# Kernel optimization log

Measured on AMD Instinct MI355X. Metric: run time of the kernel, lower is better.

## Reference

```python
import jax, jax.numpy as jnp
import numpy as np

B, C, E = 2, 128, 60000

def conv1(x, W, b):
    # pointwise conv1d: x [B,Cin,E], W [Cout,Cin], b [Cout] -> [B,Cout,E]
    return jnp.einsum('oc,bce->boe', W, x) + b[None, :, None]

def mesh_conv(x, gi, W, b):
    # MeshCNN GeMM conv: x [B,C,E], gi [B,E,4] neighbor edge ids, W [Cout,Cin,5], b [Cout]
    f = jax.vmap(lambda xb, ib: xb[:, ib])(x, gi)  # [B,C,E,4] neighbor gather
    f1, f2, f3, f4 = f[..., 0], f[..., 1], f[..., 2], f[..., 3]
    # symmetric features: [e, a+c, b+d, |a-c|, |b-d|]
    G = jnp.stack([x, f1 + f3, f2 + f4, jnp.abs(f1 - f3), jnp.abs(f2 - f4)], axis=-1)  # [B,C,E,5]
    return jnp.einsum('bces,ocs->boe', G, W) + b[None, :, None]


def setup_inputs() -> dict:
    key = jax.random.key(0)
    ks = jax.random.split(key, 16)
    s = 0.05
    return {
        'x_0': jax.random.normal(ks[0], (B, C, E), jnp.float32),
        'x_1': jax.random.normal(ks[1], (B, C, E), jnp.float32),
        'gemm': jax.random.randint(ks[2], (B, E, 4), 0, E, jnp.int32),
        'Wa_local': jax.random.normal(ks[3], (C, C), jnp.float32) * s,
        'ba_local': jax.random.normal(ks[4], (C,), jnp.float32) * s,
        'Wb_local': jax.random.normal(ks[5], (C, C), jnp.float32) * s,
        'bb_local': jax.random.normal(ks[6], (C,), jnp.float32) * s,
        'Wa_tri': jax.random.normal(ks[7], (C, C, 5), jnp.float32) * s,
        'ba_tri': jax.random.normal(ks[8], (C,), jnp.float32) * s,
        'Wb_tri': jax.random.normal(ks[9], (C, C, 5), jnp.float32) * s,
        'bb_tri': jax.random.normal(ks[10], (C,), jnp.float32) * s,
        'Wa_fuse': jax.random.normal(ks[11], (3, 2 * C), jnp.float32) * s,
        'ba_fuse': jax.random.normal(ks[12], (3,), jnp.float32) * s,
        'Wb_fuse': jax.random.normal(ks[13], (3, 2 * C), jnp.float32) * s,
        'bb_fuse': jax.random.normal(ks[14], (3,), jnp.float32) * s,
    }


def reference(x_0, x_1, gemm, Wa_local, ba_local, Wb_local, bb_local,
              Wa_tri, ba_tri, Wb_tri, bb_tri,
              Wa_fuse, ba_fuse, Wb_fuse, bb_fuse):
    a_local = conv1(x_0, Wa_local, ba_local)              # [B,C,E]
    a_tri = mesh_conv(x_0, gemm, Wa_tri, ba_tri)          # [B,C,E]
    x_a_two = jnp.concatenate([a_local, a_tri], axis=1)   # [B,2C,E]
    b_local = conv1(x_1, Wb_local, bb_local)
    b_tri = mesh_conv(x_1, gemm, Wb_tri, bb_tri)
    x_b_two = jnp.concatenate([b_local, b_tri], axis=1)
    x_a_w = conv1(x_a_two, Wa_fuse, ba_fuse)[:, None]     # [B,1,3,E]
    x_b_w = conv1(x_b_two, Wb_fuse, bb_fuse)[:, None]     # [B,1,3,E]
    return x_a_w + x_b_w
```

## Files before the change

### kernel.cpp

```cpp
#include <hip/hip_runtime.h>
#include <hip/hip_bf16.h>
#include <cstdint>

#define B_ 2
#define C_ 128
#define E_ 60000

typedef unsigned int uint32_;
typedef unsigned short ushort_;
typedef float v2f __attribute__((ext_vector_type(2)));

__device__ __forceinline__ v2f bp2(uint32_ v) {
    v2f r;
    r.x = __uint_as_float(v << 16);
    r.y = __uint_as_float(v & 0xffff0000u);
    return r;
}

__device__ __forceinline__ v2f vabs2(v2f a) {
    v2f r; r.x = fabsf(a.x); r.y = fabsf(a.y); return r;
}

__device__ __forceinline__ ushort_ f2b(float f) {
    union { float f; uint32_ u; } x; x.f = f;
    uint32_ u = x.u + 0x7fffu + ((x.u >> 16) & 1u);
    return (ushort_)(u >> 16);
}

__device__ __forceinline__ float swz_add(float v, const int pat) {
    switch (pat) {
    case 1:  return v + __int_as_float(__builtin_amdgcn_ds_swizzle(__float_as_int(v), 0x041F));
    case 2:  return v + __int_as_float(__builtin_amdgcn_ds_swizzle(__float_as_int(v), 0x081F));
    case 4:  return v + __int_as_float(__builtin_amdgcn_ds_swizzle(__float_as_int(v), 0x101F));
    case 8:  return v + __int_as_float(__builtin_amdgcn_ds_swizzle(__float_as_int(v), 0x201F));
    default: return v + __int_as_float(__builtin_amdgcn_ds_swizzle(__float_as_int(v), 0x401F));
    }
}

__global__ __launch_bounds__(256) void prep_kernel(
    const float* __restrict__ x0, const float* __restrict__ x1,
    const float* __restrict__ Wa_local, const float* __restrict__ ba_local,
    const float* __restrict__ Wb_local, const float* __restrict__ bb_local,
    const float* __restrict__ Wa_tri,  const float* __restrict__ ba_tri,
    const float* __restrict__ Wb_tri,  const float* __restrict__ bb_tri,
    const float* __restrict__ Wa_fuse, const float* __restrict__ ba_fuse,
    const float* __restrict__ Wb_fuse, const float* __restrict__ bb_fuse,
    ushort_* __restrict__ xt, float* __restrict__ Vw, float* __restrict__ cst)
{
    __shared__ float smem[32 * 65];
    const int lane = threadIdx.x & 63;
    const int wv   = threadIdx.x >> 6;

    if (blockIdx.x < 60) {
        const int pj    = blockIdx.x / 10;
        const int chunk = blockIdx.x % 10;
        const int p = pj / 3, j = pj % 3;
        const int f = chunk * 64 + lane;
        const float* Wf = p ? Wb_fuse : Wa_fuse;
        const float* Wt = p ? Wb_tri  : Wa_tri;
        const float* Wl = p ? Wb_local : Wa_local;
        const int o0 = wv * 32;
        float a0 = 0.f, a1 = 0.f, a2 = 0.f, a3 = 0.f;
        for (int o = o0; o < o0 + 32; o += 4) {
            a0 += Wf[j * 256 + 128 + o]     * Wt[(o)     * 640 + f];
            a1 += Wf[j * 256 + 129 + o]     * Wt[(o + 1) * 640 + f];
            a2 += Wf[j * 256 + 130 + o]     * Wt[(o + 2) * 640 + f];
            a3 += Wf[j * 256 + 131 + o]     * Wt[(o + 3) * 640 + f];
        }
        float acc = (a0 + a1) + (a2 + a3);
        const int s = f % 5, c = f / 5;
        if (s == 0) {
            float b0 = 0.f, b1 = 0.f, b2 = 0.f, b3 = 0.f;
            for (int o = o0; o < o0 + 32; o += 4) {
                b0 += Wf[j * 256 + o]     * Wl[(o)     * C_ + c];
                b1 += Wf[j * 256 + o + 1] * Wl[(o + 1) * C_ + c];
                b2 += Wf[j * 256 + o + 2] * Wl[(o + 2) * C_ + c];
                b3 += Wf[j * 256 + o + 3] * Wl[(o + 3) * C_ + c];
            }
            acc += (b0 + b1) + (b2 + b3);
        }
        smem[wv * 64 + lane] = acc;
        __syncthreads();
        if (wv == 0) {
            float tot = smem[lane] + smem[64 + lane] + smem[128 + lane] + smem[192 + lane];
            Vw[(pj * 5 + s) * C_ + c] = tot;
        }
    } else if (blockIdx.x == 60) {
        const int j = wv;
        if (j < 3) {
            float acc;
            {
                const int l = lane;
                acc = Wa_fuse[j * 256 + l]       * ba_local[l]
                    + Wa_fuse[j * 256 + 128 + l] * ba_tri[l]
                    + Wb_fuse[j * 256 + l]       * bb_local[l]
                    + Wb_fuse[j * 256 + 128 + l] * bb_tri[l];
            }
            {
                const int l = lane + 64;
                acc += Wa_fuse[j * 256 + l]       * ba_local[l]
                     + Wa_fuse[j * 256 + 128 + l] * ba_tri[l]
                     + Wb_fuse[j * 256 + l]       * bb_local[l]
                     + Wb_fuse[j * 256 + 128 + l] * bb_tri[l];
            }
            acc = swz_add(acc, 1); acc = swz_add(acc, 2); acc = swz_add(acc, 4);
            acc = swz_add(acc, 8); acc = swz_add(acc, 16);
            acc += __shfl_xor(acc, 32, 64);
            if (lane == 0) cst[j] = acc + ba_fuse[j] + bb_fuse[j];
        }
    } else {
        const int tb = blockIdx.x - 61;
        const int bx = tb % 1875;
        const int rz = tb / 1875;
        const int by = rz & 1;
        const int bz = rz >> 1;
        const int which = bz >> 1;
        const int b     = bz & 1;
        const float* src = (which ? x1 : x0) + (size_t)b * C_ * E_;
        const int e0 = bx * 32;
        const int c0 = by * 64;
        const int t  = threadIdx.x;
        float (*tile)[65] = (float(*)[65])smem;
        {
            const int c  = t >> 2;
            const int e8 = (t & 3) * 8;
            const float* pp = src + (size_t)(c0 + c) * E_ + e0 + e8;
            float4 v0 = *(const float4*)pp;
            float4 v1 = *(const float4*)(pp + 4);
            tile[e8 + 0][c] = v0.x; tile[e8 + 1][c] = v0.y;
            tile[e8 + 2][c] = v0.z; tile[e8 + 3][c] = v0.w;
            tile[e8 + 4][c] = v1.x; tile[e8 + 5][c] = v1.y;
            tile[e8 + 6][c] = v1.z; tile[e8 + 7][c] = v1.w;
        }
        __syncthreads();
        {
            const int e  = t >> 3;
            const int c8 = (t & 7) * 8;
            const float* r = &tile[e][c8];
            uint32_ w0 = (uint32_)f2b(r[0]) | ((uint32_)f2b(r[1]) << 16);
            uint32_ w1 = (uint32_)f2b(r[2]) | ((uint32_)f2b(r[3]) << 16);
            uint32_ w2 = (uint32_)f2b(r[4]) | ((uint32_)f2b(r[5]) << 16);
            uint32_ w3 = (uint32_)f2b(r[6]) | ((uint32_)f2b(r[7]) << 16);
            uint4 w; w.x = w0; w.y = w1; w.z = w2; w.w = w3;
            const size_t rec = (size_t)((b * E_ + e0 + e) * 2 + which);
            *(uint4*)(xt + (rec << 7) + c0 + c8) = w;
        }
    }
}

struct GD {
    uint32_ A0, A1, A2, A3, A4;
    uint32_ Cc0, Cc1, Cc2, Cc3, Cc4;
    uint32_ D0, D1, D2, D3, D4;
    uint32_ F0, F1, F2, F3, F4;
};

__device__ __forceinline__ GD issue_loads(const uint32_* __restrict__ xt,
                                          int pair, int4 gA, int4 gB, int lane)
{
    const int e0 = 2 * pair;
    const uint32_ badd = (e0 >= E_) ? (uint32_)E_ : 0u;
    const uint32_ sA = ((uint32_)e0 << 7) + lane;
    const uint32_ sB = sA + 128;
    const uint32_ n1 = ((badd + (uint32_)gA.x) << 7) + lane;
    const uint32_ n2 = ((badd + (uint32_)gA.y) << 7) + lane;
    const uint32_ n3 = ((badd + (uint32_)gA.z) << 7) + lane;
    const uint32_ n4 = ((badd + (uint32_)gA.w) << 7) + lane;
    const uint32_ m1 = ((badd + (uint32_)gB.x) << 7) + lane;
    const uint32_ m2 = ((badd + (uint32_)gB.y) << 7) + lane;
    const uint32_ m3 = ((badd + (uint32_)gB.z) << 7) + lane;
    const uint32_ m4 = ((badd + (uint32_)gB.w) << 7) + lane;
    GD g;
    g.A0 = xt[sA]; g.Cc0 = xt[sA + 64];
    g.A1 = xt[n1]; g.Cc1 = xt[n1 + 64];
    g.A2 = xt[n2]; g.Cc2 = xt[n2 + 64];
    g.A3 = xt[n3]; g.Cc3 = xt[n3 + 64];
    g.A4 = xt[n4]; g.Cc4 = xt[n4 + 64];
    g.D0 = xt[sB]; g.F0 = xt[sB + 64];
    g.D1 = xt[m1]; g.F1 = xt[m1 + 64];
    g.D2 = xt[m2]; g.F2 = xt[m2 + 64];
    g.D3 = xt[m3]; g.F3 = xt[m3 + 64];
    g.D4 = xt[m4]; g.F4 = xt[m4 + 64];
    return g;
}

__device__ __forceinline__ void edge3(uint32_ X0, uint32_ X1, uint32_ X2, uint32_ X3, uint32_ X4,
                                      uint32_ Y0, uint32_ Y1, uint32_ Y2, uint32_ Y3, uint32_ Y4,
                                      const v2f (*w)[3][5],
                                      float& r0, float& r1, float& r2)
{
    v2f a0 = bp2(X0), a1 = bp2(X1), a2 = bp2(X2), a3 = bp2(X3), a4 = bp2(X4);
    v2f b0 = bp2(Y0), b1 = bp2(Y1), b2 = bp2(Y2), b3 = bp2(Y3), b4 = bp2(Y4);
    v2f sa1 = a1 + a3, sa2 = a2 + a4;
    v2f da1 = vabs2(a1 - a3), da2 = vabs2(a2 - a4);
    v2f sb1 = b1 + b3, sb2 = b2 + b4;
    v2f db1 = vabs2(b1 - b3), db2 = vabs2(b2 - b4);
    v2f t0 = w[0][0][0] * a0, t1 = w[0][1][0] * a0, t2 = w[0][2][0] * a0;
    t0 += w[0][0][1] * sa1; t1 += w[0][1][1] * sa1; t2 += w[0][2][1] * sa1;
    t0 += w[0][0][2] * sa2; t1 += w[0][1][2] * sa2; t2 += w[0][2][2] * sa2;
    t0 += w[0][0][3] * da1; t1 += w[0][1][3] * da1; t2 += w[0][2][3] * da1;
    t0 += w[0][0][4] * da2; t1 += w[0][1][4] * da2; t2 += w[0][2][4] * da2;
    t0 += w[1][0][0] * b0;  t1 += w[1][1][0] * b0;  t2 += w[1][2][0] * b0;
    t0 += w[1][0][1] * sb1; t1 += w[1][1][1] * sb1; t2 += w[1][2][1] * sb1;
    t0 += w[1][0][2] * sb2; t1 += w[1][1][2] * sb2; t2 += w[1][2][2] * sb2;
    t0 += w[1][0][3] * db1; t1 += w[1][1][3] * db1; t2 += w[1][2][3] * db1;
    t0 += w[1][0][4] * db2; t1 += w[1][1][4] * db2; t2 += w[1][2][4] * db2;
    r0 = t0.x + t0.y; r1 = t1.x + t1.y; r2 = t2.x + t2.y;
}

__global__ __launch_bounds__(256, 3) void mesh_fused_kernel(
    const uint32_* __restrict__ xt, const int* __restrict__ gemm,
    const float* __restrict__ Vw, const float* __restrict__ cst,
    float* __restrict__ out)
{
    const int lane = threadIdx.x & 63;
    const int wv   = threadIdx.x >> 6;
    const int gw   = blockIdx.x * 4 + wv;
    const int nw   = gridDim.x * 4;

    v2f w[2][3][5];
#pragma unroll
    for (int p = 0; p < 2; ++p)
#pragma unroll
        for (int j = 0; j < 3; ++j)
#pragma unroll
            for (int s = 0; s < 5; ++s)
                w[p][j][s] = *(const v2f*)(Vw + (((p * 3 + j) * 5 + s) << 7) + lane * 2);

    const int  jj     = lane >> 4;
    const bool is0    = (jj == 0), is1 = (jj == 1);
    const bool writer = ((lane & 15) == 0) && (jj < 3);
    const float cj    = is0 ? cst[0] : (is1 ? cst[1] : cst[2]);
    float* obase      = out + (size_t)(jj < 3 ? jj : 2) * E_;

    const int4* g4 = (const int4*)gemm;
    const int npair = (B_ * E_) / 2;

    int pnext = (gw + nw < npair) ? gw + nw : gw;
    int4 giA = g4[2 * gw], giB = g4[2 * gw + 1];
    GD cur = issue_loads(xt, gw, giA, giB, lane);
    int4 niA = g4[2 * pnext], niB = g4[2 * pnext + 1];

#pragma unroll 2
    for (int pair = gw; pair < npair; pair += nw) {
        GD nb = issue_loads(xt, pnext, niA, niB, lane);
        const int p2 = (pnext + nw < npair) ? pnext + nw : pnext;
        niA = g4[2 * p2]; niB = g4[2 * p2 + 1];

        float rA0, rA1, rA2, rB0, rB1, rB2;
        edge3(cur.A0, cur.A1, cur.A2, cur.A3, cur.A4,
              cur.Cc0, cur.Cc1, cur.Cc2, cur.Cc3, cur.Cc4, w, rA0, rA1, rA2);
        edge3(cur.D0, cur.D1, cur.D2, cur.D3, cur.D4,
              cur.F0, cur.F1, cur.F2, cur.F3, cur.F4, w, rB0, rB1, rB2);

        rA0 = swz_add(rA0, 16); rB0 = swz_add(rB0, 16);
        rA1 = swz_add(rA1, 16); rB1 = swz_add(rB1, 16);
        rA2 = swz_add(rA2, 16); rB2 = swz_add(rB2, 16);
        rA0 += __shfl_xor(rA0, 32, 64); rB0 += __shfl_xor(rB0, 32, 64);
        rA1 += __shfl_xor(rA1, 32, 64); rB1 += __shfl_xor(rB1, 32, 64);
        rA2 += __shfl_xor(rA2, 32, 64); rB2 += __shfl_xor(rB2, 32, 64);

        float vA = is0 ? rA0 : (is1 ? rA1 : rA2);
        float vB = is0 ? rB0 : (is1 ? rB1 : rB2);
        vA = swz_add(vA, 1); vB = swz_add(vB, 1);
        vA = swz_add(vA, 2); vB = swz_add(vB, 2);
        vA = swz_add(vA, 4); vB = swz_add(vB, 4);
        vA = swz_add(vA, 8); vB = swz_add(vB, 8);

        if (writer) {
            const int e0p = 2 * pair;
            const int bb  = (e0p >= E_) ? 1 : 0;
            const int ee  = e0p - (bb ? E_ : 0);
            float2 st; st.x = vA + cj; st.y = vB + cj;
            *(float2*)(obase + (bb ? 3 * E_ : 0) + ee) = st;
        }

        cur = nb;
        pnext = p2;
    }
}

extern "C" void kernel_launch(void* const* d_in, const int* in_sizes, int n_in,
                              void* d_out, int out_size, void* d_ws, size_t ws_size,
                              hipStream_t stream) {
    const float* x0       = (const float*)d_in[0];
    const float* x1       = (const float*)d_in[1];
    const int*   gemm     = (const int*)d_in[2];
    const float* Wa_local = (const float*)d_in[3];
    const float* ba_local = (const float*)d_in[4];
    const float* Wb_local = (const float*)d_in[5];
    const float* bb_local = (const float*)d_in[6];
    const float* Wa_tri   = (const float*)d_in[7];
    const float* ba_tri   = (const float*)d_in[8];
    const float* Wb_tri   = (const float*)d_in[9];
    const float* bb_tri   = (const float*)d_in[10];
    const float* Wa_fuse  = (const float*)d_in[11];
    const float* ba_fuse  = (const float*)d_in[12];
    const float* Wb_fuse  = (const float*)d_in[13];
    const float* bb_fuse  = (const float*)d_in[14];
    float* out = (float*)d_out;

    ushort_* xt  = (ushort_*)d_ws;
    float*   Vw  = (float*)(xt + (size_t)B_ * E_ * 2 * C_);
    float*   cst = Vw + 2 * 3 * 5 * C_;

    hipLaunchKernelGGL(prep_kernel, dim3(61 + 15000), dim3(256), 0, stream,
                       x0, x1,
                       Wa_local, ba_local, Wb_local, bb_local,
                       Wa_tri, ba_tri, Wb_tri, bb_tri,
                       Wa_fuse, ba_fuse, Wb_fuse, bb_fuse, xt, Vw, cst);

    hipLaunchKernelGGL(mesh_fused_kernel, dim3(2048), dim3(256), 0, stream,
                       (const uint32_*)xt, gemm, Vw, cst, out);
}
```

Before: 214.8 us.

## Restructure transpose blocks to cover both inputs and all channels per tile

The prep transpose now has each block handle 32 edges across all 128 channels of both x0 and x1, converting to bf16 before staging in shared memory with a padded row stride. Each block then writes whole 512-byte records with four 16-byte stores. This cuts the block count from 15000 to 3750 and halves shared-memory traffic, at the cost of strided 128-byte global reads per thread. A sched_barrier is also added in the main loop to keep prefetch loads from being interleaved with compute.

```diff
diff --git a/kernel.cpp b/kernel.cpp
--- a/kernel.cpp
+++ b/kernel.cpp
@@ -36,6 +36,8 @@
     default: return v + __int_as_float(__builtin_amdgcn_ds_swizzle(__float_as_int(v), 0x401F));
     }
 }
+
+#define RS_ 264
 
 __global__ __launch_bounds__(256) void prep_kernel(
     const float* __restrict__ x0, const float* __restrict__ x1,
@@ -47,11 +49,12 @@
     const float* __restrict__ Wb_fuse, const float* __restrict__ bb_fuse,
     ushort_* __restrict__ xt, float* __restrict__ Vw, float* __restrict__ cst)
 {
-    __shared__ float smem[32 * 65];
+    __shared__ __align__(16) ushort_ smem_us[32 * RS_];
     const int lane = threadIdx.x & 63;
     const int wv   = threadIdx.x >> 6;
 
     if (blockIdx.x < 60) {
+        float* smemf = (float*)smem_us;
         const int pj    = blockIdx.x / 10;
         const int chunk = blockIdx.x % 10;
         const int p = pj / 3, j = pj % 3;
@@ -79,10 +82,10 @@
             }
             acc += (b0 + b1) + (b2 + b3);
         }
-        smem[wv * 64 + lane] = acc;
+        smemf[wv * 64 + lane] = acc;
         __syncthreads();
         if (wv == 0) {
-            float tot = smem[lane] + smem[64 + lane] + smem[128 + lane] + smem[192 + lane];
+            float tot = smemf[lane] + smemf[64 + lane] + smemf[128 + lane] + smemf[192 + lane];
             Vw[(pj * 5 + s) * C_ + c] = tot;
         }
     } else if (blockIdx.x == 60) {
@@ -110,41 +113,36 @@
         }
     } else {
         const int tb = blockIdx.x - 61;
+        const int b  = tb / 1875;
         const int bx = tb % 1875;
-        const int rz = tb / 1875;
-        const int by = rz & 1;
-        const int bz = rz >> 1;
-        const int which = bz >> 1;
-        const int b     = bz & 1;
-        const float* src = (which ? x1 : x0) + (size_t)b * C_ * E_;
         const int e0 = bx * 32;
-        const int c0 = by * 64;
         const int t  = threadIdx.x;
-        float (*tile)[65] = (float(*)[65])smem;
-        {
-            const int c  = t >> 2;
-            const int e8 = (t & 3) * 8;
-            const float* pp = src + (size_t)(c0 + c) * E_ + e0 + e8;
-            float4 v0 = *(const float4*)pp;
-            float4 v1 = *(const float4*)(pp + 4);
-            tile[e8 + 0][c] = v0.x; tile[e8 + 1][c] = v0.y;
-            tile[e8 + 2][c] = v0.z; tile[e8 + 3][c] = v0.w;
-            tile[e8 + 4][c] = v1.x; tile[e8 + 5][c] = v1.y;
-            tile[e8 + 6][c] = v1.z; tile[e8 + 7][c] = v1.w;
+        const int which = t >> 7;
+        const int c     = t & 127;
+        const float* src = (which ? x1 : x0) + ((size_t)b * C_ + c) * E_ + e0;
+        float4 v[8];
+#pragma unroll
+        for (int k = 0; k < 8; ++k) v[k] = ((const float4*)src)[k];
+#pragma unroll
+        for (int k = 0; k < 8; ++k) {
+            smem_us[(4 * k + 0) * RS_ + t] = f2b(v[k].x);
+            smem_us[(4 * k + 1) * RS_ + t] = f2b(v[k].y);
+            smem_us[(4 * k + 2) * RS_ + t] = f2b(v[k].z);
+            smem_us[(4 * k + 3) * RS_ + t] = f2b(v[k].w);
         }
         __syncthreads();
-        {
-            const int e  = t >> 3;
-            const int c8 = (t & 7) * 8;
-            const float* r = &tile[e][c8];
-            uint32_ w0 = (uint32_)f2b(r[0]) | ((uint32_)f2b(r[1]) << 16);
-            uint32_ w1 = (uint32_)f2b(r[2]) | ((uint32_)f2b(r[3]) << 16);
-            uint32_ w2 = (uint32_)f2b(r[4]) | ((uint32_)f2b(r[5]) << 16);
-            uint32_ w3 = (uint32_)f2b(r[6]) | ((uint32_)f2b(r[7]) << 16);
-            uint4 w; w.x = w0; w.y = w1; w.z = w2; w.w = w3;
-            const size_t rec = (size_t)((b * E_ + e0 + e) * 2 + which);
-            *(uint4*)(xt + (rec << 7) + c0 + c8) = w;
-        }
+        const int e  = t >> 3;
+        const int u0 = (t & 7) * 32;
+        const ushort_* r = smem_us + e * RS_ + u0;
+        uint4 w0 = *(const uint4*)(r);
+        uint4 w1 = *(const uint4*)(r + 8);
+        uint4 w2 = *(const uint4*)(r + 16);
+        uint4 w3 = *(const uint4*)(r + 24);
+        ushort_* dst = xt + ((size_t)(b * E_ + e0 + e) << 8) + u0;
+        ((uint4*)dst)[0] = w0;
+        ((uint4*)dst)[1] = w1;
+        ((uint4*)dst)[2] = w2;
+        ((uint4*)dst)[3] = w3;
     }
 }
 
@@ -247,6 +245,8 @@
         const int p2 = (pnext + nw < npair) ? pnext + nw : pnext;
         niA = g4[2 * p2]; niB = g4[2 * p2 + 1];
 
+        __builtin_amdgcn_sched_barrier(0);
+
         float rA0, rA1, rA2, rB0, rB1, rB2;
         edge3(cur.A0, cur.A1, cur.A2, cur.A3, cur.A4,
               cur.Cc0, cur.Cc1, cur.Cc2, cur.Cc3, cur.Cc4, w, rA0, rA1, rA2);
@@ -304,7 +304,7 @@
     float*   Vw  = (float*)(xt + (size_t)B_ * E_ * 2 * C_);
     float*   cst = Vw + 2 * 3 * 5 * C_;
 
-    hipLaunchKernelGGL(prep_kernel, dim3(61 + 15000), dim3(256), 0, stream,
+    hipLaunchKernelGGL(prep_kernel, dim3(61 + 2 * (E_ / 32)), dim3(256), 0, stream,
                        x0, x1,
                        Wa_local, ba_local, Wb_local, bb_local,
                        Wa_tri, ba_tri, Wb_tri, bb_tri,
```

Result: slower. 225.0 us (+4.7%).

## Split bf16 transposed features into channel halves and gather in two passes

Applied to the files above, without the earlier changes.

The bf16 transposed feature buffer is split into two channel halves (lo/hi), each holding 64 channels for both inputs per edge. The fused gather kernel becomes a half kernel launched twice: the first pass writes partial outputs and the second adds its contribution plus the constant. Each pass has half the working set, so random neighbor gathers are more likely to hit in cache. Each wave now handles four edges per iteration without software prefetch. The cost is an extra launch, a read-modify-write of the output, and a second read of the gather indices.

```diff
diff --git a/kernel.cpp b/kernel.cpp
--- a/kernel.cpp
+++ b/kernel.cpp
@@ -45,7 +45,8 @@
     const float* __restrict__ Wb_tri,  const float* __restrict__ bb_tri,
     const float* __restrict__ Wa_fuse, const float* __restrict__ ba_fuse,
     const float* __restrict__ Wb_fuse, const float* __restrict__ bb_fuse,
-    ushort_* __restrict__ xt, float* __restrict__ Vw, float* __restrict__ cst)
+    ushort_* __restrict__ xt_lo, ushort_* __restrict__ xt_hi,
+    float* __restrict__ Vw, float* __restrict__ cst)
 {
     __shared__ float smem[32 * 65];
     const int lane = threadIdx.x & 63;
@@ -117,6 +118,7 @@
         const int which = bz >> 1;
         const int b     = bz & 1;
         const float* src = (which ? x1 : x0) + (size_t)b * C_ * E_;
+        ushort_* half_base = by ? xt_hi : xt_lo;
         const int e0 = bx * 32;
         const int c0 = by * 64;
         const int t  = threadIdx.x;
@@ -142,90 +144,29 @@
             uint32_ w2 = (uint32_)f2b(r[4]) | ((uint32_)f2b(r[5]) << 16);
             uint32_ w3 = (uint32_)f2b(r[6]) | ((uint32_)f2b(r[7]) << 16);
             uint4 w; w.x = w0; w.y = w1; w.z = w2; w.w = w3;
-            const size_t rec = (size_t)((b * E_ + e0 + e) * 2 + which);
-            *(uint4*)(xt + (rec << 7) + c0 + c8) = w;
+            const size_t rec = (size_t)(b * E_ + e0 + e) * 2 + which;
+            *(uint4*)(half_base + (rec << 6) + c8) = w;
         }
     }
 }
 
-struct GD {
-    uint32_ A0, A1, A2, A3, A4;
-    uint32_ Cc0, Cc1, Cc2, Cc3, Cc4;
-    uint32_ D0, D1, D2, D3, D4;
-    uint32_ F0, F1, F2, F3, F4;
-};
-
-__device__ __forceinline__ GD issue_loads(const uint32_* __restrict__ xt,
-                                          int pair, int4 gA, int4 gB, int lane)
-{
-    const int e0 = 2 * pair;
-    const uint32_ badd = (e0 >= E_) ? (uint32_)E_ : 0u;
-    const uint32_ sA = ((uint32_)e0 << 7) + lane;
-    const uint32_ sB = sA + 128;
-    const uint32_ n1 = ((badd + (uint32_)gA.x) << 7) + lane;
-    const uint32_ n2 = ((badd + (uint32_)gA.y) << 7) + lane;
-    const uint32_ n3 = ((badd + (uint32_)gA.z) << 7) + lane;
-    const uint32_ n4 = ((badd + (uint32_)gA.w) << 7) + lane;
-    const uint32_ m1 = ((badd + (uint32_)gB.x) << 7) + lane;
-    const uint32_ m2 = ((badd + (uint32_)gB.y) << 7) + lane;
-    const uint32_ m3 = ((badd + (uint32_)gB.z) << 7) + lane;
-    const uint32_ m4 = ((badd + (uint32_)gB.w) << 7) + lane;
-    GD g;
-    g.A0 = xt[sA]; g.Cc0 = xt[sA + 64];
-    g.A1 = xt[n1]; g.Cc1 = xt[n1 + 64];
-    g.A2 = xt[n2]; g.Cc2 = xt[n2 + 64];
-    g.A3 = xt[n3]; g.Cc3 = xt[n3 + 64];
-    g.A4 = xt[n4]; g.Cc4 = xt[n4 + 64];
-    g.D0 = xt[sB]; g.F0 = xt[sB + 64];
-    g.D1 = xt[m1]; g.F1 = xt[m1 + 64];
-    g.D2 = xt[m2]; g.F2 = xt[m2 + 64];
-    g.D3 = xt[m3]; g.F3 = xt[m3 + 64];
-    g.D4 = xt[m4]; g.F4 = xt[m4 + 64];
-    return g;
-}
-
-__device__ __forceinline__ void edge3(uint32_ X0, uint32_ X1, uint32_ X2, uint32_ X3, uint32_ X4,
-                                      uint32_ Y0, uint32_ Y1, uint32_ Y2, uint32_ Y3, uint32_ Y4,
-                                      const v2f (*w)[3][5],
-                                      float& r0, float& r1, float& r2)
-{
-    v2f a0 = bp2(X0), a1 = bp2(X1), a2 = bp2(X2), a3 = bp2(X3), a4 = bp2(X4);
-    v2f b0 = bp2(Y0), b1 = bp2(Y1), b2 = bp2(Y2), b3 = bp2(Y3), b4 = bp2(Y4);
-    v2f sa1 = a1 + a3, sa2 = a2 + a4;
-    v2f da1 = vabs2(a1 - a3), da2 = vabs2(a2 - a4);
-    v2f sb1 = b1 + b3, sb2 = b2 + b4;
-    v2f db1 = vabs2(b1 - b3), db2 = vabs2(b2 - b4);
-    v2f t0 = w[0][0][0] * a0, t1 = w[0][1][0] * a0, t2 = w[0][2][0] * a0;
-    t0 += w[0][0][1] * sa1; t1 += w[0][1][1] * sa1; t2 += w[0][2][1] * sa1;
-    t0 += w[0][0][2] * sa2; t1 += w[0][1][2] * sa2; t2 += w[0][2][2] * sa2;
-    t0 += w[0][0][3] * da1; t1 += w[0][1][3] * da1; t2 += w[0][2][3] * da1;
-    t0 += w[0][0][4] * da2; t1 += w[0][1][4] * da2; t2 += w[0][2][4] * da2;
-    t0 += w[1][0][0] * b0;  t1 += w[1][1][0] * b0;  t2 += w[1][2][0] * b0;
-    t0 += w[1][0][1] * sb1; t1 += w[1][1][1] * sb1; t2 += w[1][2][1] * sb1;
-    t0 += w[1][0][2] * sb2; t1 += w[1][1][2] * sb2; t2 += w[1][2][2] * sb2;
-    t0 += w[1][0][3] * db1; t1 += w[1][1][3] * db1; t2 += w[1][2][3] * db1;
-    t0 += w[1][0][4] * db2; t1 += w[1][1][4] * db2; t2 += w[1][2][4] * db2;
-    r0 = t0.x + t0.y; r1 = t1.x + t1.y; r2 = t2.x + t2.y;
-}
-
-__global__ __launch_bounds__(256, 3) void mesh_fused_kernel(
-    const uint32_* __restrict__ xt, const int* __restrict__ gemm,
+__global__ __launch_bounds__(256, 3) void mesh_half_kernel(
+    const uint32_* __restrict__ xh, const int* __restrict__ gemm,
     const float* __restrict__ Vw, const float* __restrict__ cst,
-    float* __restrict__ out)
+    float* __restrict__ out, const int coff, const int finalp)
 {
     const int lane = threadIdx.x & 63;
     const int wv   = threadIdx.x >> 6;
     const int gw   = blockIdx.x * 4 + wv;
     const int nw   = gridDim.x * 4;
 
-    v2f w[2][3][5];
-#pragma unroll
-    for (int p = 0; p < 2; ++p)
-#pragma unroll
-        for (int j = 0; j < 3; ++j)
-#pragma unroll
-            for (int s = 0; s < 5; ++s)
-                w[p][j][s] = *(const v2f*)(Vw + (((p * 3 + j) * 5 + s) << 7) + lane * 2);
+    const int p = lane >> 5;
+    v2f w[3][5];
+#pragma unroll
+    for (int j = 0; j < 3; ++j)
+#pragma unroll
+        for (int s = 0; s < 5; ++s)
+            w[j][s] = *(const v2f*)(Vw + ((p * 3 + j) * 5 + s) * C_ + coff + (lane & 31) * 2);
 
     const int  jj     = lane >> 4;
     const bool is0    = (jj == 0), is1 = (jj == 1);
@@ -234,49 +175,80 @@
     float* obase      = out + (size_t)(jj < 3 ? jj : 2) * E_;
 
     const int4* g4 = (const int4*)gemm;
-    const int npair = (B_ * E_) / 2;
-
-    int pnext = (gw + nw < npair) ? gw + nw : gw;
-    int4 giA = g4[2 * gw], giB = g4[2 * gw + 1];
-    GD cur = issue_loads(xt, gw, giA, giB, lane);
-    int4 niA = g4[2 * pnext], niB = g4[2 * pnext + 1];
-
-#pragma unroll 2
-    for (int pair = gw; pair < npair; pair += nw) {
-        GD nb = issue_loads(xt, pnext, niA, niB, lane);
-        const int p2 = (pnext + nw < npair) ? pnext + nw : pnext;
-        niA = g4[2 * p2]; niB = g4[2 * p2 + 1];
-
-        float rA0, rA1, rA2, rB0, rB1, rB2;
-        edge3(cur.A0, cur.A1, cur.A2, cur.A3, cur.A4,
-              cur.Cc0, cur.Cc1, cur.Cc2, cur.Cc3, cur.Cc4, w, rA0, rA1, rA2);
-        edge3(cur.D0, cur.D1, cur.D2, cur.D3, cur.D4,
-              cur.F0, cur.F1, cur.F2, cur.F3, cur.F4, w, rB0, rB1, rB2);
-
-        rA0 = swz_add(rA0, 16); rB0 = swz_add(rB0, 16);
-        rA1 = swz_add(rA1, 16); rB1 = swz_add(rB1, 16);
-        rA2 = swz_add(rA2, 16); rB2 = swz_add(rB2, 16);
-        rA0 += __shfl_xor(rA0, 32, 64); rB0 += __shfl_xor(rB0, 32, 64);
-        rA1 += __shfl_xor(rA1, 32, 64); rB1 += __shfl_xor(rB1, 32, 64);
-        rA2 += __shfl_xor(rA2, 32, 64); rB2 += __shfl_xor(rB2, 32, 64);
-
-        float vA = is0 ? rA0 : (is1 ? rA1 : rA2);
-        float vB = is0 ? rB0 : (is1 ? rB1 : rB2);
-        vA = swz_add(vA, 1); vB = swz_add(vB, 1);
-        vA = swz_add(vA, 2); vB = swz_add(vB, 2);
-        vA = swz_add(vA, 4); vB = swz_add(vB, 4);
-        vA = swz_add(vA, 8); vB = swz_add(vB, 8);
+    const int nquad = (B_ * E_) / 4;
+
+    for (int q = gw; q < nquad; q += nw) {
+        const int e0g = 4 * q;
+        const int b   = (e0g >= E_) ? 1 : 0;
+        const uint32_ badd = b ? (uint32_)E_ : 0u;
+
+        const int4 g0 = g4[e0g], g1 = g4[e0g + 1], g2 = g4[e0g + 2], g3 = g4[e0g + 3];
+
+        uint32_ S[4], N1[4], N2[4], N3[4], N4[4];
+#pragma unroll
+        for (int k = 0; k < 4; ++k)
+            S[k] = xh[(((uint32_)(e0g + k)) << 6) + lane];
+        N1[0] = xh[((badd + (uint32_)g0.x) << 6) + lane];
+        N2[0] = xh[((badd + (uint32_)g0.y) << 6) + lane];
+        N3[0] = xh[((badd + (uint32_)g0.z) << 6) + lane];
+        N4[0] = xh[((badd + (uint32_)g0.w) << 6) + lane];
+        N1[1] = xh[((badd + (uint32_)g1.x) << 6) + lane];
+        N2[1] = xh[((badd + (uint32_)g1.y) << 6) + lane];
+        N3[1] = xh[((badd + (uint32_)g1.z) << 6) + lane];
+        N4[1] = xh[((badd + (uint32_)g1.w) << 6) + lane];
+        N1[2] = xh[((badd + (uint32_)g2.x) << 6) + lane];
+        N2[2] = xh[((badd + (uint32_)g2.y) << 6) + lane];
+        N3[2] = xh[((badd + (uint32_)g2.z) << 6) + lane];
+        N4[2] = xh[((badd + (uint32_)g2.w) << 6) + lane];
+        N1[3] = xh[((badd + (uint32_)g3.x) << 6) + lane];
+        N2[3] = xh[((badd + (uint32_)g3.y) << 6) + lane];
+        N3[3] = xh[((badd + (uint32_)g3.z) << 6) + lane];
+        N4[3] = xh[((badd + (uint32_)g3.w) << 6) + lane];
+
+        float r0[4], r1[4], r2[4];
+#pragma unroll
+        for (int k = 0; k < 4; ++k) {
+            v2f a0 = bp2(S[k]);
+            v2f a1 = bp2(N1[k]), a2 = bp2(N2[k]), a3 = bp2(N3[k]), a4 = bp2(N4[k]);
+            v2f s1 = a1 + a3, s2 = a2 + a4;
+            v2f d1 = vabs2(a1 - a3), d2 = vabs2(a2 - a4);
+            v2f t0 = w[0][0] * a0, t1 = w[1][0] * a0, t2 = w[2][0] * a0;
+            t0 += w[0][1] * s1; t1 += w[1][1] * s1; t2 += w[2][1] * s1;
+            t0 += w[0][2] * s2; t1 += w[1][2] * s2; t2 += w[2][2] * s2;
+            t0 += w[0][3] * d1; t1 += w[1][3] * d1; t2 += w[2][3] * d1;
+            t0 += w[0][4] * d2; t1 += w[1][4] * d2; t2 += w[2][4] * d2;
+            r0[k] = t0.x + t0.y; r1[k] = t1.x + t1.y; r2[k] = t2.x + t2.y;
+        }
+
+#pragma unroll
+        for (int k = 0; k < 4; ++k) {
+            r0[k] = swz_add(r0[k], 16); r1[k] = swz_add(r1[k], 16); r2[k] = swz_add(r2[k], 16);
+            r0[k] += __shfl_xor(r0[k], 32, 64);
+            r1[k] += __shfl_xor(r1[k], 32, 64);
+            r2[k] += __shfl_xor(r2[k], 32, 64);
+        }
+        float v0 = is0 ? r0[0] : (is1 ? r1[0] : r2[0]);
+        float v1 = is0 ? r0[1] : (is1 ? r1[1] : r2[1]);
+        float v2 = is0 ? r0[2] : (is1 ? r1[2] : r2[2]);
+        float v3 = is0 ? r0[3] : (is1 ? r1[3] : r2[3]);
+        v0 = swz_add(v0, 1); v1 = swz_add(v1, 1); v2 = swz_add(v2, 1); v3 = swz_add(v3, 1);
+        v0 = swz_add(v0, 2); v1 = swz_add(v1, 2); v2 = swz_add(v2, 2); v3 = swz_add(v3, 2);
+        v0 = swz_add(v0, 4); v1 = swz_add(v1, 4); v2 = swz_add(v2, 4); v3 = swz_add(v3, 4);
+        v0 = swz_add(v0, 8); v1 = swz_add(v1, 8); v2 = swz_add(v2, 8); v3 = swz_add(v3, 8);
 
         if (writer) {
-            const int e0p = 2 * pair;
-            const int bb  = (e0p >= E_) ? 1 : 0;
-            const int ee  = e0p - (bb ? E_ : 0);
-            float2 st; st.x = vA + cj; st.y = vB + cj;
-            *(float2*)(obase + (bb ? 3 * E_ : 0) + ee) = st;
-        }
-
-        cur = nb;
-        pnext = p2;
+            const int el = e0g - (int)badd;
+            float* dst = obase + (b ? 3 * E_ : 0) + el;
+            float4 st;
+            if (finalp) {
+                float4 old = *(const float4*)dst;
+                st.x = old.x + v0 + cj; st.y = old.y + v1 + cj;
+                st.z = old.z + v2 + cj; st.w = old.w + v3 + cj;
+            } else {
+                st.x = v0; st.y = v1; st.z = v2; st.w = v3;
+            }
+            *(float4*)dst = st;
+        }
     }
 }
 
@@ -300,16 +272,19 @@
     const float* bb_fuse  = (const float*)d_in[14];
     float* out = (float*)d_out;
 
-    ushort_* xt  = (ushort_*)d_ws;
-    float*   Vw  = (float*)(xt + (size_t)B_ * E_ * 2 * C_);
-    float*   cst = Vw + 2 * 3 * 5 * C_;
-
-    hipLaunchKernelGGL(prep_kernel, dim3(61 + 15000), dim3(256), 0, stream,
+    ushort_* xt_lo = (ushort_*)d_ws;
+    ushort_* xt_hi = xt_lo + (size_t)B_ * E_ * 128;
+    float*   Vw    = (float*)(xt_hi + (size_t)B_ * E_ * 128);
+    float*   cst   = Vw + 2 * 3 * 5 * C_;
+
+    hipLaunchKernelGGL(prep_kernel, dim3(61 + 8 * (E_ / 32)), dim3(256), 0, stream,
                        x0, x1,
                        Wa_local, ba_local, Wb_local, bb_local,
                        Wa_tri, ba_tri, Wb_tri, bb_tri,
-                       Wa_fuse, ba_fuse, Wb_fuse, bb_fuse, xt, Vw, cst);
-
-    hipLaunchKernelGGL(mesh_fused_kernel, dim3(2048), dim3(256), 0, stream,
-                       (const uint32_*)xt, gemm, Vw, cst, out);
-}
+                       Wa_fuse, ba_fuse, Wb_fuse, bb_fuse, xt_lo, xt_hi, Vw, cst);
+
+    hipLaunchKernelGGL(mesh_half_kernel, dim3(2048), dim3(256), 0, stream,
+                       (const uint32_*)xt_lo, gemm, Vw, cst, out, 0, 0);
+    hipLaunchKernelGGL(mesh_half_kernel, dim3(2048), dim3(256), 0, stream,
+                       (const uint32_*)xt_hi, gemm, Vw, cst, out, 64, 1);
+}
```

Result: no change. 218.4 us (+1.6%).

## Remap lanes to four channels with 8-byte gathers and drop software prefetch

Applied to the files above, without the earlier changes.

Each lane now covers four bf16 channels of one input, selected by the lane half, instead of two channels of both inputs. The gathers become 8-byte uint2 loads, which halves the number of load instructions and the per-lane weight registers. The explicit double-buffered prefetch of the next pair's neighbour data is removed; only the index prefetch is kept. Launch bounds are raised to 4 blocks per unit, relying on higher occupancy to hide gather latency instead of prefetching, which risks exposed latency if occupancy does not rise.

```diff
diff --git a/kernel.cpp b/kernel.cpp
--- a/kernel.cpp
+++ b/kernel.cpp
@@ -9,6 +9,7 @@
 typedef unsigned int uint32_;
 typedef unsigned short ushort_;
 typedef float v2f __attribute__((ext_vector_type(2)));
+typedef float v4f __attribute__((ext_vector_type(4)));
 
 __device__ __forceinline__ v2f bp2(uint32_ v) {
     v2f r;
@@ -17,8 +18,18 @@
     return r;
 }
 
-__device__ __forceinline__ v2f vabs2(v2f a) {
-    v2f r; r.x = fabsf(a.x); r.y = fabsf(a.y); return r;
+__device__ __forceinline__ v4f bp4(uint2 v) {
+    v4f r;
+    r.x = __uint_as_float(v.x << 16);
+    r.y = __uint_as_float(v.x & 0xffff0000u);
+    r.z = __uint_as_float(v.y << 16);
+    r.w = __uint_as_float(v.y & 0xffff0000u);
+    return r;
+}
+
+__device__ __forceinline__ v4f vabs4(v4f a) {
+    v4f r; r.x = fabsf(a.x); r.y = fabsf(a.y); r.z = fabsf(a.z); r.w = fabsf(a.w);
+    return r;
 }
 
 __device__ __forceinline__ ushort_ f2b(float f) {
@@ -148,68 +159,8 @@
     }
 }
 
-struct GD {
-    uint32_ A0, A1, A2, A3, A4;
-    uint32_ Cc0, Cc1, Cc2, Cc3, Cc4;
-    uint32_ D0, D1, D2, D3, D4;
-    uint32_ F0, F1, F2, F3, F4;
-};
-
-__device__ __forceinline__ GD issue_loads(const uint32_* __restrict__ xt,
-                                          int pair, int4 gA, int4 gB, int lane)
-{
-    const int e0 = 2 * pair;
-    const uint32_ badd = (e0 >= E_) ? (uint32_)E_ : 0u;
-    const uint32_ sA = ((uint32_)e0 << 7) + lane;
-    const uint32_ sB = sA + 128;
-    const uint32_ n1 = ((badd + (uint32_)gA.x) << 7) + lane;
-    const uint32_ n2 = ((badd + (uint32_)gA.y) << 7) + lane;
-    const uint32_ n3 = ((badd + (uint32_)gA.z) << 7) + lane;
-    const uint32_ n4 = ((badd + (uint32_)gA.w) << 7) + lane;
-    const uint32_ m1 = ((badd + (uint32_)gB.x) << 7) + lane;
-    const uint32_ m2 = ((badd + (uint32_)gB.y) << 7) + lane;
-    const uint32_ m3 = ((badd + (uint32_)gB.z) << 7) + lane;
-    const uint32_ m4 = ((badd + (uint32_)gB.w) << 7) + lane;
-    GD g;
-    g.A0 = xt[sA]; g.Cc0 = xt[sA + 64];
-    g.A1 = xt[n1]; g.Cc1 = xt[n1 + 64];
-    g.A2 = xt[n2]; g.Cc2 = xt[n2 + 64];
-    g.A3 = xt[n3]; g.Cc3 = xt[n3 + 64];
-    g.A4 = xt[n4]; g.Cc4 = xt[n4 + 64];
-    g.D0 = xt[sB]; g.F0 = xt[sB + 64];
-    g.D1 = xt[m1]; g.F1 = xt[m1 + 64];
-    g.D2 = xt[m2]; g.F2 = xt[m2 + 64];
-    g.D3 = xt[m3]; g.F3 = xt[m3 + 64];
-    g.D4 = xt[m4]; g.F4 = xt[m4 + 64];
-    return g;
-}
-
-__device__ __forceinline__ void edge3(uint32_ X0, uint32_ X1, uint32_ X2, uint32_ X3, uint32_ X4,
-                                      uint32_ Y0, uint32_ Y1, uint32_ Y2, uint32_ Y3, uint32_ Y4,
-                                      const v2f (*w)[3][5],
-                                      float& r0, float& r1, float& r2)
-{
-    v2f a0 = bp2(X0), a1 = bp2(X1), a2 = bp2(X2), a3 = bp2(X3), a4 = bp2(X4);
-    v2f b0 = bp2(Y0), b1 = bp2(Y1), b2 = bp2(Y2), b3 = bp2(Y3), b4 = bp2(Y4);
-    v2f sa1 = a1 + a3, sa2 = a2 + a4;
-    v2f da1 = vabs2(a1 - a3), da2 = vabs2(a2 - a4);
-    v2f sb1 = b1 + b3, sb2 = b2 + b4;
-    v2f db1 = vabs2(b1 - b3), db2 = vabs2(b2 - b4);
-    v2f t0 = w[0][0][0] * a0, t1 = w[0][1][0] * a0, t2 = w[0][2][0] * a0;
-    t0 += w[0][0][1] * sa1; t1 += w[0][1][1] * sa1; t2 += w[0][2][1] * sa1;
-    t0 += w[0][0][2] * sa2; t1 += w[0][1][2] * sa2; t2 += w[0][2][2] * sa2;
-    t0 += w[0][0][3] * da1; t1 += w[0][1][3] * da1; t2 += w[0][2][3] * da1;
-    t0 += w[0][0][4] * da2; t1 += w[0][1][4] * da2; t2 += w[0][2][4] * da2;
-    t0 += w[1][0][0] * b0;  t1 += w[1][1][0] * b0;  t2 += w[1][2][0] * b0;
-    t0 += w[1][0][1] * sb1; t1 += w[1][1][1] * sb1; t2 += w[1][2][1] * sb1;
-    t0 += w[1][0][2] * sb2; t1 += w[1][1][2] * sb2; t2 += w[1][2][2] * sb2;
-    t0 += w[1][0][3] * db1; t1 += w[1][1][3] * db1; t2 += w[1][2][3] * db1;
-    t0 += w[1][0][4] * db2; t1 += w[1][1][4] * db2; t2 += w[1][2][4] * db2;
-    r0 = t0.x + t0.y; r1 = t1.x + t1.y; r2 = t2.x + t2.y;
-}
-
-__global__ __launch_bounds__(256, 3) void mesh_fused_kernel(
-    const uint32_* __restrict__ xt, const int* __restrict__ gemm,
+__global__ __launch_bounds__(256, 4) void mesh_fused_kernel(
+    const uint2* __restrict__ xt2, const int* __restrict__ gemm,
     const float* __restrict__ Vw, const float* __restrict__ cst,
     float* __restrict__ out)
 {
@@ -218,14 +169,14 @@
     const int gw   = blockIdx.x * 4 + wv;
     const int nw   = gridDim.x * 4;
 
-    v2f w[2][3][5];
+    const int p  = lane >> 5;
+    const int c4 = (lane & 31) * 4;
+    v4f w[3][5];
 #pragma unroll
-    for (int p = 0; p < 2; ++p)
+    for (int j = 0; j < 3; ++j)
 #pragma unroll
-        for (int j = 0; j < 3; ++j)
-#pragma unroll
-            for (int s = 0; s < 5; ++s)
-                w[p][j][s] = *(const v2f*)(Vw + (((p * 3 + j) * 5 + s) << 7) + lane * 2);
+        for (int s = 0; s < 5; ++s)
+            w[j][s] = *(const v4f*)(Vw + ((p * 3 + j) * 5 + s) * C_ + c4);
 
     const int  jj     = lane >> 4;
     const bool is0    = (jj == 0), is1 = (jj == 1);
@@ -236,22 +187,57 @@
     const int4* g4 = (const int4*)gemm;
     const int npair = (B_ * E_) / 2;
 
-    int pnext = (gw + nw < npair) ? gw + nw : gw;
     int4 giA = g4[2 * gw], giB = g4[2 * gw + 1];
-    GD cur = issue_loads(xt, gw, giA, giB, lane);
-    int4 niA = g4[2 * pnext], niB = g4[2 * pnext + 1];
-
-#pragma unroll 2
+
     for (int pair = gw; pair < npair; pair += nw) {
-        GD nb = issue_loads(xt, pnext, niA, niB, lane);
-        const int p2 = (pnext + nw < npair) ? pnext + nw : pnext;
-        niA = g4[2 * p2]; niB = g4[2 * p2 + 1];
-
-        float rA0, rA1, rA2, rB0, rB1, rB2;
-        edge3(cur.A0, cur.A1, cur.A2, cur.A3, cur.A4,
-              cur.Cc0, cur.Cc1, cur.Cc2, cur.Cc3, cur.Cc4, w, rA0, rA1, rA2);
-        edge3(cur.D0, cur.D1, cur.D2, cur.D3, cur.D4,
-              cur.F0, cur.F1, cur.F2, cur.F3, cur.F4, w, rB0, rB1, rB2);
+        const int nxt = pair + nw;
+        const int4 gA = giA, gB = giB;
+        if (nxt < npair) { giA = g4[2 * nxt]; giB = g4[2 * nxt + 1]; }
+
+        const int e0 = 2 * pair;
+        const uint32_ badd = (e0 >= E_) ? (uint32_)E_ : 0u;
+
+        const uint2 SA = xt2[(((uint32_)e0)     << 6) + lane];
+        const uint2 SB = xt2[(((uint32_)e0 + 1) << 6) + lane];
+        const uint2 A1 = xt2[((badd + (uint32_)gA.x) << 6) + lane];
+        const uint2 A2 = xt2[((badd + (uint32_)gA.y) << 6) + lane];
+        const uint2 A3 = xt2[((badd + (uint32_)gA.z) << 6) + lane];
+        const uint2 A4 = xt2[((badd + (uint32_)gA.w) << 6) + lane];
+        const uint2 B1 = xt2[((badd + (uint32_)gB.x) << 6) + lane];
+        const uint2 B2 = xt2[((badd + (uint32_)gB.y) << 6) + lane];
+        const uint2 B3 = xt2[((badd + (uint32_)gB.z) << 6) + lane];
+        const uint2 B4 = xt2[((badd + (uint32_)gB.w) << 6) + lane];
+
+        float rA0, rA1, rA2;
+        {
+            v4f a0 = bp4(SA);
+            v4f a1 = bp4(A1), a2 = bp4(A2), a3 = bp4(A3), a4 = bp4(A4);
+            v4f s1 = a1 + a3, s2 = a2 + a4;
+            v4f d1 = vabs4(a1 - a3), d2 = vabs4(a2 - a4);
+            v4f t0 = w[0][0] * a0, t1 = w[1][0] * a0, t2 = w[2][0] * a0;
+            t0 += w[0][1] * s1; t1 += w[1][1] * s1; t2 += w[2][1] * s1;
+            t0 += w[0][2] * s2; t1 += w[1][2] * s2; t2 += w[2][2] * s2;
+            t0 += w[0][3] * d1; t1 += w[1][3] * d1; t2 += w[2][3] * d1;
+            t0 += w[0][4] * d2; t1 += w[1][4] * d2; t2 += w[2][4] * d2;
+            rA0 = (t0.x + t0.y) + (t0.z + t0.w);
+            rA1 = (t1.x + t1.y) + (t1.z + t1.w);
+            rA2 = (t2.x + t2.y) + (t2.z + t2.w);
+        }
+        float rB0, rB1, rB2;
+        {
+            v4f a0 = bp4(SB);
+            v4f a1 = bp4(B1), a2 = bp4(B2), a3 = bp4(B3), a4 = bp4(B4);
+            v4f s1 = a1 + a3, s2 = a2 + a4;
+            v4f d1 = vabs4(a1 - a3), d2 = vabs4(a2 - a4);
+            v4f t0 = w[0][0] * a0, t1 = w[1][0] * a0, t2 = w[2][0] * a0;
+            t0 += w[0][1] * s1; t1 += w[1][1] * s1; t2 += w[2][1] * s1;
+            t0 += w[0][2] * s2; t1 += w[1][2] * s2; t2 += w[2][2] * s2;
+            t0 += w[0][3] * d1; t1 += w[1][3] * d1; t2 += w[2][3] * d1;
+            t0 += w[0][4] * d2; t1 += w[1][4] * d2; t2 += w[2][4] * d2;
+            rB0 = (t0.x + t0.y) + (t0.z + t0.w);
+            rB1 = (t1.x + t1.y) + (t1.z + t1.w);
+            rB2 = (t2.x + t2.y) + (t2.z + t2.w);
+        }
 
         rA0 = swz_add(rA0, 16); rB0 = swz_add(rB0, 16);
         rA1 = swz_add(rA1, 16); rB1 = swz_add(rB1, 16);
@@ -268,15 +254,11 @@
         vA = swz_add(vA, 8); vB = swz_add(vB, 8);
 
         if (writer) {
-            const int e0p = 2 * pair;
-            const int bb  = (e0p >= E_) ? 1 : 0;
-            const int ee  = e0p - (bb ? E_ : 0);
+            const int bb = (e0 >= E_) ? 1 : 0;
+            const int ee = e0 - (bb ? E_ : 0);
             float2 st; st.x = vA + cj; st.y = vB + cj;
             *(float2*)(obase + (bb ? 3 * E_ : 0) + ee) = st;
         }
-
-        cur = nb;
-        pnext = p2;
     }
 }
 
@@ -304,12 +286,12 @@
     float*   Vw  = (float*)(xt + (size_t)B_ * E_ * 2 * C_);
     float*   cst = Vw + 2 * 3 * 5 * C_;
 
-    hipLaunchKernelGGL(prep_kernel, dim3(61 + 15000), dim3(256), 0, stream,
+    hipLaunchKernelGGL(prep_kernel, dim3(61 + 8 * (E_ / 32)), dim3(256), 0, stream,
                        x0, x1,
                        Wa_local, ba_local, Wb_local, bb_local,
                        Wa_tri, ba_tri, Wb_tri, bb_tri,
                        Wa_fuse, ba_fuse, Wb_fuse, bb_fuse, xt, Vw, cst);
 
     hipLaunchKernelGGL(mesh_fused_kernel, dim3(2048), dim3(256), 0, stream,
-                       (const uint32_*)xt, gemm, Vw, cst, out);
-}
+                       (const uint2*)xt, gemm, Vw, cst, out);
+}
```

Result: no change. 213.6 us (-0.6%).
